# Optimization experiments

Measured on AMD Instinct MI355X. Metric: run time of the kernel, lower is better.

## Reference

```python
import jax, jax.numpy as jnp
import numpy as np

HEADS = 4
SIZE = 3


def setup_inputs() -> dict:
    key = jax.random.key(0)
    ks = jax.random.split(key, 8)
    B, C, D, H, W = 2, 64, 24, 24, 24
    s = 1.0 / np.sqrt(C)
    x = jax.random.normal(ks[0], (B, C, D, H, W), jnp.float32)
    cemb = jax.random.normal(ks[1], (B, C), jnp.float32)
    Wq = jax.random.normal(ks[2], (C, C), jnp.float32) * s
    bq = jax.random.normal(ks[3], (C,), jnp.float32) * 0.01
    Wk = jax.random.normal(ks[4], (C, C), jnp.float32) * s
    bk = jax.random.normal(ks[5], (C,), jnp.float32) * 0.01
    Wv = jax.random.normal(ks[6], (C, C), jnp.float32) * s
    bv = jax.random.normal(ks[7], (C,), jnp.float32) * 0.01
    return {"x": x, "cemb": cemb, "Wq": Wq, "bq": bq, "Wk": Wk, "bk": bk, "Wv": Wv, "bv": bv}


def _unfold(t, size, heads):
    # t: (B, D, H, W, C) -> (B, D*H*W, heads, size^3, C//heads), zero padded borders
    B, D, H, W, C = t.shape
    pad = size // 2
    tp = jnp.pad(t, ((0, 0), (pad, pad), (pad, pad), (pad, pad), (0, 0)))
    # depth shift outermost, then height, then width (matches torch unfold order)
    patches = jnp.stack(
        [tp[:, i:i + D, j:j + H, l:l + W, :]
         for i in range(size) for j in range(size) for l in range(size)],
        axis=4)  # (B, D, H, W, ws, C)
    ws = size ** 3
    hd = C // heads
    return patches.reshape(B, D * H * W, ws, heads, hd).transpose(0, 1, 3, 2, 4)


def reference(x, cemb, Wq, bq, Wk, bk, Wv, bv):
    # x: (B, C, D, H, W); cemb unused by the original forward
    B, C, D, H, W = x.shape
    heads, size = HEADS, SIZE
    hd = C // heads
    xc = jnp.transpose(x, (0, 2, 3, 4, 1))  # (B, D, H, W, C)
    q = xc @ Wq.T + bq
    k = xc @ Wk.T + bk
    v = xc @ Wv.T + bv
    kw = _unfold(k, size, heads)  # (B, N, h, ws, hd)
    vw = _unfold(v, size, heads)
    qh = q.reshape(B, D * H * W, heads, 1, hd) * (hd ** -0.5)
    attn = jnp.einsum('bnhqd,bnhkd->bnhqk', qh, kw)  # (B, N, h, 1, ws)
    attn = jax.nn.softmax(attn, axis=-1)
    h = jnp.einsum('bnhqk,bnhkd->bnhqd', attn, vw).reshape(B, D, H, W, C)
    out = xc + h
    return jnp.transpose(out, (0, 4, 1, 2, 3))
```

## Files before the change

### kernel.cpp

```cpp
#include <hip/hip_runtime.h>

#define NV 13824
#define CCH 64
#define NB 2

__global__ __launch_bounds__(256) void qkv_kernel(
    const float* __restrict__ x,
    const float* __restrict__ Wq, const float* __restrict__ bq,
    const float* __restrict__ Wk, const float* __restrict__ bk,
    const float* __restrict__ Wv, const float* __restrict__ bv,
    float* __restrict__ qo, float* __restrict__ ko, float* __restrict__ vo)
{
    __shared__ float sW[3 * 4096];
    __shared__ float sB[3 * 64];
    const int t = threadIdx.x;

    {
        const float4* s0 = (const float4*)Wq;
        const float4* s1 = (const float4*)Wk;
        const float4* s2 = (const float4*)Wv;
        float4* d = (float4*)sW;
        for (int i = t; i < 1024; i += 256) {
            d[i]        = s0[i];
            d[1024 + i] = s1[i];
            d[2048 + i] = s2[i];
        }
        if (t < 64) { sB[t] = bq[t]; sB[64 + t] = bk[t]; sB[128 + t] = bv[t]; }
    }
    __syncthreads();

    const int row  = t & 63;
    const int part = t >> 6;
    const int gr   = blockIdx.x * 64 + row;
    const int b    = gr / NV;
    const int n    = gr - b * NV;

    const float* xb = x + (size_t)b * CCH * NV + n;

    float4 xr[16];
    #pragma unroll
    for (int c4 = 0; c4 < 16; ++c4) {
        xr[c4].x = xb[(size_t)(c4 * 4 + 0) * NV];
        xr[c4].y = xb[(size_t)(c4 * 4 + 1) * NV];
        xr[c4].z = xb[(size_t)(c4 * 4 + 2) * NV];
        xr[c4].w = xb[(size_t)(c4 * 4 + 3) * NV];
    }

    const float4* wq = (const float4*)(sW + (size_t)(part * 16) * 64);
    const float4* wk = (const float4*)(sW + 4096 + (size_t)(part * 16) * 64);
    const float4* wv = (const float4*)(sW + 8192 + (size_t)(part * 16) * 64);

    float* qd = qo + (size_t)gr * 64 + part * 16;
    float* kd = ko + (size_t)gr * 64 + part * 16;
    float* vd = vo + (size_t)gr * 64 + part * 16;

    for (int oo = 0; oo < 16; ++oo) {
        float aq = 0.f, ak = 0.f, av = 0.f;
        #pragma unroll
        for (int c4 = 0; c4 < 16; ++c4) {
            const float4 xv = xr[c4];
            const float4 a = wq[oo * 16 + c4];
            aq += xv.x * a.x + xv.y * a.y + xv.z * a.z + xv.w * a.w;
            const float4 bb = wk[oo * 16 + c4];
            ak += xv.x * bb.x + xv.y * bb.y + xv.z * bb.z + xv.w * bb.w;
            const float4 cc = wv[oo * 16 + c4];
            av += xv.x * cc.x + xv.y * cc.y + xv.z * cc.z + xv.w * cc.w;
        }
        qd[oo] = aq + sB[part * 16 + oo];
        kd[oo] = ak + sB[64 + part * 16 + oo];
        vd[oo] = av + sB[128 + part * 16 + oo];
    }
}

__global__ __launch_bounds__(256) void attn_kernel(
    const float* __restrict__ x,
    const float* __restrict__ qw,
    const float* __restrict__ kw,
    const float* __restrict__ vw,
    float* __restrict__ out)
{
    const int t    = threadIdx.x;
    const int vb   = t >> 2;
    const int head = t & 3;
    const int gr   = blockIdx.x * 64 + vb;
    const int b    = gr / NV;
    const int n    = gr - b * NV;
    const int d    = n / 576;
    const int rem  = n - d * 576;
    const int r    = rem / 24;
    const int w    = rem - r * 24;

    int nidx[27];
    #pragma unroll
    for (int i3 = 0; i3 < 3; ++i3)
    #pragma unroll
    for (int j3 = 0; j3 < 3; ++j3)
    #pragma unroll
    for (int l3 = 0; l3 < 3; ++l3) {
        const int dd = d + i3 - 1;
        const int rr = r + j3 - 1;
        const int ww = w + l3 - 1;
        const bool ok = ((unsigned)dd < 24u) & ((unsigned)rr < 24u) & ((unsigned)ww < 24u);
        nidx[(i3 * 3 + j3) * 3 + l3] = ok ? ((dd * 24 + rr) * 24 + ww) : -1;
    }

    const float4* qp = (const float4*)(qw + (size_t)gr * 64 + head * 16);
    float4 q0 = qp[0], q1 = qp[1], q2 = qp[2], q3 = qp[3];
    const float s = 0.25f;
    q0.x *= s; q0.y *= s; q0.z *= s; q0.w *= s;
    q1.x *= s; q1.y *= s; q1.z *= s; q1.w *= s;
    q2.x *= s; q2.y *= s; q2.z *= s; q2.w *= s;
    q3.x *= s; q3.y *= s; q3.z *= s; q3.w *= s;

    const float* kbase = kw + (size_t)b * NV * 64 + head * 16;

    float logit[27];
    #pragma unroll
    for (int j = 0; j < 27; ++j) {
        float a = 0.f;
        if (nidx[j] >= 0) {
            const float4* kp = (const float4*)(kbase + (size_t)nidx[j] * 64);
            const float4 k0 = kp[0], k1 = kp[1], k2 = kp[2], k3 = kp[3];
            a  = q0.x * k0.x + q0.y * k0.y + q0.z * k0.z + q0.w * k0.w;
            a += q1.x * k1.x + q1.y * k1.y + q1.z * k1.z + q1.w * k1.w;
            a += q2.x * k2.x + q2.y * k2.y + q2.z * k2.z + q2.w * k2.w;
            a += q3.x * k3.x + q3.y * k3.y + q3.z * k3.z + q3.w * k3.w;
        }
        logit[j] = a;
    }

    float m = logit[0];
    #pragma unroll
    for (int j = 1; j < 27; ++j) m = fmaxf(m, logit[j]);
    float ssum = 0.f;
    #pragma unroll
    for (int j = 0; j < 27; ++j) {
        const float e = __expf(logit[j] - m);
        logit[j] = e;
        ssum += e;
    }
    const float inv = 1.f / ssum;

    float a00=0.f,a01=0.f,a02=0.f,a03=0.f, a10=0.f,a11=0.f,a12=0.f,a13=0.f;
    float a20=0.f,a21=0.f,a22=0.f,a23=0.f, a30=0.f,a31=0.f,a32=0.f,a33=0.f;
    const float* vbase = vw + (size_t)b * NV * 64 + head * 16;
    #pragma unroll
    for (int j = 0; j < 27; ++j) {
        if (nidx[j] >= 0) {
            const float p = logit[j];
            const float4* vp = (const float4*)(vbase + (size_t)nidx[j] * 64);
            const float4 v0 = vp[0], v1 = vp[1], v2 = vp[2], v3 = vp[3];
            a00 += p * v0.x; a01 += p * v0.y; a02 += p * v0.z; a03 += p * v0.w;
            a10 += p * v1.x; a11 += p * v1.y; a12 += p * v1.z; a13 += p * v1.w;
            a20 += p * v2.x; a21 += p * v2.y; a22 += p * v2.z; a23 += p * v2.w;
            a30 += p * v3.x; a31 += p * v3.y; a32 += p * v3.z; a33 += p * v3.w;
        }
    }

    const size_t cb = (size_t)b * CCH * NV + (size_t)(head * 16) * NV + n;
    const float* xb = x + cb;
    float* ob = out + cb;
    float av[16] = {a00,a01,a02,a03,a10,a11,a12,a13,a20,a21,a22,a23,a30,a31,a32,a33};
    #pragma unroll
    for (int i = 0; i < 16; ++i) {
        ob[(size_t)i * NV] = xb[(size_t)i * NV] + av[i] * inv;
    }
}

extern "C" void kernel_launch(void* const* d_in, const int* in_sizes, int n_in,
                              void* d_out, int out_size, void* d_ws, size_t ws_size,
                              hipStream_t stream) {
    const float* x  = (const float*)d_in[0];
    const float* Wq = (const float*)d_in[2];
    const float* bq = (const float*)d_in[3];
    const float* Wk = (const float*)d_in[4];
    const float* bk = (const float*)d_in[5];
    const float* Wv = (const float*)d_in[6];
    const float* bv = (const float*)d_in[7];
    float* out = (float*)d_out;

    float* ws = (float*)d_ws;
    const size_t RC = (size_t)NB * NV * CCH;
    float* q = ws;
    float* k = ws + RC;
    float* v = ws + 2 * RC;

    const int nrows = NB * NV;
    const int blocks = nrows / 64;

    qkv_kernel<<<blocks, 256, 0, stream>>>(x, Wq, bq, Wk, bk, Wv, bv, q, k, v);
    attn_kernel<<<blocks, 256, 0, stream>>>(x, q, k, v, out);
}
```

Baseline: 132.2 us.

## Register-tile QKV projection via shared memory and split attention heads across lane pairs

The QKV kernel now stages a 64x128 tile of x in shared memory with coalesced float4 loads and keeps transposed weights in shared memory. Each thread computes a 4-row by 8-column register tile for all three projections and writes float4 outputs. The attention kernel splits each head's 16 channels across two lanes, combining the partial dot products with a shuffle, which doubles the thread count and cuts per-thread register use. The larger shared memory footprint (about 80KB per block) may limit occupancy in the QKV kernel.

```diff
diff --git a/kernel.cpp b/kernel.cpp
--- a/kernel.cpp
+++ b/kernel.cpp
@@ -11,64 +11,84 @@
     const float* __restrict__ Wv, const float* __restrict__ bv,
     float* __restrict__ qo, float* __restrict__ ko, float* __restrict__ vo)
 {
-    __shared__ float sW[3 * 4096];
-    __shared__ float sB[3 * 64];
-    const int t = threadIdx.x;
+    __shared__ float sX[64 * 128];
+    __shared__ float sWT[3 * 64 * 64];
+
+    const int t  = threadIdx.x;
+    const int n0 = blockIdx.x * 128;
+    const int b  = n0 / NV;
+    const int nn = n0 - b * NV;
 
     {
-        const float4* s0 = (const float4*)Wq;
-        const float4* s1 = (const float4*)Wk;
-        const float4* s2 = (const float4*)Wv;
-        float4* d = (float4*)sW;
-        for (int i = t; i < 1024; i += 256) {
-            d[i]        = s0[i];
-            d[1024 + i] = s1[i];
-            d[2048 + i] = s2[i];
-        }
-        if (t < 64) { sB[t] = bq[t]; sB[64 + t] = bk[t]; sB[128 + t] = bv[t]; }
+        const float* xb = x + (size_t)b * CCH * NV + nn;
+        float4* dst = (float4*)sX;
+        #pragma unroll
+        for (int it = 0; it < 8; ++it) {
+            const int i = it * 256 + t;
+            const int c = i >> 5;
+            const int f = i & 31;
+            dst[i] = *(const float4*)(xb + (size_t)c * NV + f * 4);
+        }
+    }
+    {
+        const int o  = t & 63;
+        const int kk = t >> 6;
+        const float* const Ws[3] = {Wq, Wk, Wv};
+        #pragma unroll
+        for (int m = 0; m < 3; ++m) {
+            const float* wm = Ws[m] + o * 64 + kk * 16;
+            float* dd = sWT + m * 4096 + o;
+            #pragma unroll
+            for (int k2 = 0; k2 < 16; ++k2)
+                dd[(kk * 16 + k2) * 64] = wm[k2];
+        }
     }
     __syncthreads();
 
-    const int row  = t & 63;
-    const int part = t >> 6;
-    const int gr   = blockIdx.x * 64 + row;
-    const int b    = gr / NV;
-    const int n    = gr - b * NV;
-
-    const float* xb = x + (size_t)b * CCH * NV + n;
-
-    float4 xr[16];
-    #pragma unroll
-    for (int c4 = 0; c4 < 16; ++c4) {
-        xr[c4].x = xb[(size_t)(c4 * 4 + 0) * NV];
-        xr[c4].y = xb[(size_t)(c4 * 4 + 1) * NV];
-        xr[c4].z = xb[(size_t)(c4 * 4 + 2) * NV];
-        xr[c4].w = xb[(size_t)(c4 * 4 + 3) * NV];
-    }
-
-    const float4* wq = (const float4*)(sW + (size_t)(part * 16) * 64);
-    const float4* wk = (const float4*)(sW + 4096 + (size_t)(part * 16) * 64);
-    const float4* wv = (const float4*)(sW + 8192 + (size_t)(part * 16) * 64);
-
-    float* qd = qo + (size_t)gr * 64 + part * 16;
-    float* kd = ko + (size_t)gr * 64 + part * 16;
-    float* vd = vo + (size_t)gr * 64 + part * 16;
-
-    for (int oo = 0; oo < 16; ++oo) {
-        float aq = 0.f, ak = 0.f, av = 0.f;
-        #pragma unroll
-        for (int c4 = 0; c4 < 16; ++c4) {
-            const float4 xv = xr[c4];
-            const float4 a = wq[oo * 16 + c4];
-            aq += xv.x * a.x + xv.y * a.y + xv.z * a.z + xv.w * a.w;
-            const float4 bb = wk[oo * 16 + c4];
-            ak += xv.x * bb.x + xv.y * bb.y + xv.z * bb.z + xv.w * bb.w;
-            const float4 cc = wv[oo * 16 + c4];
-            av += xv.x * cc.x + xv.y * cc.y + xv.z * cc.z + xv.w * cc.w;
-        }
-        qd[oo] = aq + sB[part * 16 + oo];
-        kd[oo] = ak + sB[64 + part * 16 + oo];
-        vd[oo] = av + sB[128 + part * 16 + oo];
+    const int c0 = (t & 7) * 8;
+    const int r0 = (t >> 3) * 4;
+
+    float4 acc[3][8];
+    #pragma unroll
+    for (int m = 0; m < 3; ++m)
+        #pragma unroll
+        for (int c = 0; c < 8; ++c)
+            acc[m][c] = make_float4(0.f, 0.f, 0.f, 0.f);
+
+#define QKV_FMA(A, S) { (A).x += a.x*(S); (A).y += a.y*(S); (A).z += a.z*(S); (A).w += a.w*(S); }
+
+    #pragma unroll 4
+    for (int k = 0; k < 64; ++k) {
+        const float4 a = *(const float4*)(sX + k * 128 + r0);
+        #pragma unroll
+        for (int m = 0; m < 3; ++m) {
+            const float* wrow = sWT + m * 4096 + k * 64 + c0;
+            const float4 b0 = *(const float4*)(wrow);
+            const float4 b1 = *(const float4*)(wrow + 4);
+            QKV_FMA(acc[m][0], b0.x) QKV_FMA(acc[m][1], b0.y)
+            QKV_FMA(acc[m][2], b0.z) QKV_FMA(acc[m][3], b0.w)
+            QKV_FMA(acc[m][4], b1.x) QKV_FMA(acc[m][5], b1.y)
+            QKV_FMA(acc[m][6], b1.z) QKV_FMA(acc[m][7], b1.w)
+        }
+    }
+#undef QKV_FMA
+
+    float* const outs[3] = {qo, ko, vo};
+    const float* const bs[3] = {bq, bk, bv};
+    #pragma unroll
+    for (int m = 0; m < 3; ++m) {
+        const float4 bb0 = *(const float4*)(bs[m] + c0);
+        const float4 bb1 = *(const float4*)(bs[m] + c0 + 4);
+        float* ob = outs[m] + (size_t)(n0 + r0) * 64 + c0;
+#define QKV_ROW(RR, F) { \
+        float4 o0 = make_float4(acc[m][0].F + bb0.x, acc[m][1].F + bb0.y, \
+                                acc[m][2].F + bb0.z, acc[m][3].F + bb0.w); \
+        float4 o1 = make_float4(acc[m][4].F + bb1.x, acc[m][5].F + bb1.y, \
+                                acc[m][6].F + bb1.z, acc[m][7].F + bb1.w); \
+        *(float4*)(ob + (size_t)(RR) * 64)     = o0; \
+        *(float4*)(ob + (size_t)(RR) * 64 + 4) = o1; }
+        QKV_ROW(0, x) QKV_ROW(1, y) QKV_ROW(2, z) QKV_ROW(3, w)
+#undef QKV_ROW
     }
 }
 
@@ -80,9 +100,10 @@
     float* __restrict__ out)
 {
     const int t    = threadIdx.x;
-    const int vb   = t >> 2;
-    const int head = t & 3;
-    const int gr   = blockIdx.x * 64 + vb;
+    const int half = t & 1;
+    const int head = (t >> 1) & 3;
+    const int vb   = t >> 3;
+    const int gr   = blockIdx.x * 32 + vb;
     const int b    = gr / NV;
     const int n    = gr - b * NV;
     const int d    = n / 576;
@@ -104,15 +125,15 @@
         nidx[(i3 * 3 + j3) * 3 + l3] = ok ? ((dd * 24 + rr) * 24 + ww) : -1;
     }
 
-    const float4* qp = (const float4*)(qw + (size_t)gr * 64 + head * 16);
-    float4 q0 = qp[0], q1 = qp[1], q2 = qp[2], q3 = qp[3];
+    const int coff = head * 16 + half * 8;
+
+    const float4* qp = (const float4*)(qw + (size_t)gr * 64 + coff);
+    float4 q0 = qp[0], q1 = qp[1];
     const float s = 0.25f;
     q0.x *= s; q0.y *= s; q0.z *= s; q0.w *= s;
     q1.x *= s; q1.y *= s; q1.z *= s; q1.w *= s;
-    q2.x *= s; q2.y *= s; q2.z *= s; q2.w *= s;
-    q3.x *= s; q3.y *= s; q3.z *= s; q3.w *= s;
-
-    const float* kbase = kw + (size_t)b * NV * 64 + head * 16;
+
+    const float* kbase = kw + (size_t)b * NV * 64 + coff;
 
     float logit[27];
     #pragma unroll
@@ -120,12 +141,11 @@
         float a = 0.f;
         if (nidx[j] >= 0) {
             const float4* kp = (const float4*)(kbase + (size_t)nidx[j] * 64);
-            const float4 k0 = kp[0], k1 = kp[1], k2 = kp[2], k3 = kp[3];
+            const float4 k0 = kp[0], k1 = kp[1];
             a  = q0.x * k0.x + q0.y * k0.y + q0.z * k0.z + q0.w * k0.w;
             a += q1.x * k1.x + q1.y * k1.y + q1.z * k1.z + q1.w * k1.w;
-            a += q2.x * k2.x + q2.y * k2.y + q2.z * k2.z + q2.w * k2.w;
-            a += q3.x * k3.x + q3.y * k3.y + q3.z * k3.z + q3.w * k3.w;
-        }
+        }
+        a += __shfl_xor(a, 1, 64);
         logit[j] = a;
     }
 
@@ -141,28 +161,25 @@
     }
     const float inv = 1.f / ssum;
 
-    float a00=0.f,a01=0.f,a02=0.f,a03=0.f, a10=0.f,a11=0.f,a12=0.f,a13=0.f;
-    float a20=0.f,a21=0.f,a22=0.f,a23=0.f, a30=0.f,a31=0.f,a32=0.f,a33=0.f;
-    const float* vbase = vw + (size_t)b * NV * 64 + head * 16;
+    float a0=0.f,a1=0.f,a2=0.f,a3=0.f,a4=0.f,a5=0.f,a6=0.f,a7=0.f;
+    const float* vbase = vw + (size_t)b * NV * 64 + coff;
     #pragma unroll
     for (int j = 0; j < 27; ++j) {
         if (nidx[j] >= 0) {
             const float p = logit[j];
             const float4* vp = (const float4*)(vbase + (size_t)nidx[j] * 64);
-            const float4 v0 = vp[0], v1 = vp[1], v2 = vp[2], v3 = vp[3];
-            a00 += p * v0.x; a01 += p * v0.y; a02 += p * v0.z; a03 += p * v0.w;
-            a10 += p * v1.x; a11 += p * v1.y; a12 += p * v1.z; a13 += p * v1.w;
-            a20 += p * v2.x; a21 += p * v2.y; a22 += p * v2.z; a23 += p * v2.w;
-            a30 += p * v3.x; a31 += p * v3.y; a32 += p * v3.z; a33 += p * v3.w;
-        }
-    }
-
-    const size_t cb = (size_t)b * CCH * NV + (size_t)(head * 16) * NV + n;
+            const float4 v0 = vp[0], v1 = vp[1];
+            a0 += p * v0.x; a1 += p * v0.y; a2 += p * v0.z; a3 += p * v0.w;
+            a4 += p * v1.x; a5 += p * v1.y; a6 += p * v1.z; a7 += p * v1.w;
+        }
+    }
+
+    const size_t cb = (size_t)b * CCH * NV + (size_t)coff * NV + n;
     const float* xb = x + cb;
     float* ob = out + cb;
-    float av[16] = {a00,a01,a02,a03,a10,a11,a12,a13,a20,a21,a22,a23,a30,a31,a32,a33};
-    #pragma unroll
-    for (int i = 0; i < 16; ++i) {
+    float av[8] = {a0,a1,a2,a3,a4,a5,a6,a7};
+    #pragma unroll
+    for (int i = 0; i < 8; ++i) {
         ob[(size_t)i * NV] = xb[(size_t)i * NV] + av[i] * inv;
     }
 }
@@ -186,8 +203,7 @@
     float* v = ws + 2 * RC;
 
     const int nrows = NB * NV;
-    const int blocks = nrows / 64;
-
-    qkv_kernel<<<blocks, 256, 0, stream>>>(x, Wq, bq, Wk, bk, Wv, bv, q, k, v);
-    attn_kernel<<<blocks, 256, 0, stream>>>(x, q, k, v, out);
+
+    qkv_kernel<<<nrows / 128, 256, 0, stream>>>(x, Wq, bq, Wk, bk, Wv, bv, q, k, v);
+    attn_kernel<<<nrows / 32, 256, 0, stream>>>(x, q, k, v, out);
 }
```

After: 114.3 us. -13.5%, faster.
